# Kernel optimization log

Measured on AMD Instinct MI355X. Metric: run time of the kernel, lower is better.

The kernel has to match this reference:

```python
import jax, jax.numpy as jnp
import numpy as np

B, D, O, K = 8192, 256, 256, 16


def setup_inputs() -> dict:
    key = jax.random.key(0)
    k1, k2, k3, k4 = jax.random.split(key, 4)
    x = jax.random.normal(k1, (B, D), dtype=jnp.float32)
    # learned params
    values = jax.random.uniform(k2, (O, D, K), dtype=jnp.float32, minval=-0.05, maxval=0.05)
    skip_w = jax.random.normal(k3, (O, D), dtype=jnp.float32) * (1.0 / np.sqrt(D))
    skip_b = jax.random.uniform(k4, (O,), dtype=jnp.float32, minval=-1.0, maxval=1.0) / np.sqrt(D)
    # fixed buffer (non-trainable)
    grid = jnp.linspace(-1.0, 1.0, K).astype(jnp.float32)
    return {"x": x, "values": values, "skip_w": skip_w, "skip_b": skip_b, "grid": grid}


def reference(x, values, skip_w, skip_b, grid):
    # x: [B, D]; values: [O, D, K]; grid: [K]
    num_knots = grid.shape[0]
    xc = jnp.clip(x, -1.0, 1.0)
    # torch.bucketize(x, grid) (right=False) == searchsorted side='left'
    right = jnp.searchsorted(grid, xc, side="left")            # [B, D]
    left = jnp.clip(right - 1, 0, num_knots - 2)               # [B, D]
    right = left + 1
    g0 = grid[left]
    g1 = grid[right]
    w = (xc - g0) / (g1 - g0 + 1e-12)                          # [B, D]
    # sparse linear-interp coefficients over knots: 2 nonzeros per (b, d)
    coeff = (1.0 - w)[..., None] * jax.nn.one_hot(left, num_knots, dtype=xc.dtype) \
          + w[..., None] * jax.nn.one_hot(right, num_knots, dtype=xc.dtype)  # [B, D, K]
    # y[b,o] = sum_d sum_k coeff[b,d,k] * values[o,d,k]  (== per-dim gather+interp+accumulate)
    y = jnp.einsum("bdk,odk->bo", coeff, values)
    y = y + xc @ skip_w.T + skip_b
    return y
```

## Files before the change

kernel.cpp:

```cpp
#include <hip/hip_runtime.h>
#include <hip/hip_bf16.h>
#include <stdint.h>


#define D_DIM  256
#define O_DIM  256
#define KK     4096
#define BM     64
#define BN     64
#define BK     128
#define NT     (KK / BK)
#define NTHREADS 256

typedef __attribute__((ext_vector_type(8))) short bf16x8;
typedef __attribute__((ext_vector_type(4))) float f32x4;

__global__ __launch_bounds__(256) void kan_prep(
    const float* __restrict__ values,
    const float* __restrict__ skip_w,
    const float* __restrict__ gknots,
    unsigned short* __restrict__ Vp)
{
    int tid = blockIdx.x * blockDim.x + threadIdx.x;
    int e = tid * 8;
    int o = e >> 12;
    int kflat = e & 4095;
    int od = (o << 8) | (kflat >> 4);
    float sw = skip_w[od];
    int kmod = kflat & 15;

    const float4* vp4 = reinterpret_cast<const float4*>(values + e);
    float4 v0 = vp4[0], v1 = vp4[1];
    float f[8] = {v0.x, v0.y, v0.z, v0.w, v1.x, v1.y, v1.z, v1.w};
    unsigned int w[4];
#pragma unroll
    for (int j = 0; j < 4; ++j) {
        float2 ab;
        ab.x = f[2*j]     + gknots[kmod + 2*j]     * sw;
        ab.y = f[2*j + 1] + gknots[kmod + 2*j + 1] * sw;
        __hip_bfloat162 p2 = __float22bfloat162_rn(ab);
        __builtin_memcpy(&w[j], &p2, 4);
    }

    int cblk = o >> 6, n = o & 63;
    int kt = kflat >> 7;
    int k8 = (kflat >> 3) & 15;
    int slot = n * 16 + (k8 ^ (n & 7));
    size_t dst = (((size_t)(cblk * NT + kt)) * 1024 + (size_t)slot) * 8;
    *reinterpret_cast<uint4*>(Vp + dst) = make_uint4(w[0], w[1], w[2], w[3]);
}

__global__ __launch_bounds__(NTHREADS, 2) void kan_gemm(
    const float* __restrict__ x,
    const unsigned short* __restrict__ Vp,
    const float* __restrict__ skip_b,
    float* __restrict__ out)
{
    __shared__ unsigned short As[2][BM * BK];
    __shared__ unsigned short Bs[2][BN * BK];

    const int t    = threadIdx.x;
    const int lane = t & 63;
    const int wid  = t >> 6;
    const int wm   = wid >> 1;
    const int wn   = wid & 1;
    const int l15  = lane & 15;
    const int lhi  = lane >> 4;

    const int bm0  = (int)(blockIdx.x >> 2) * BM;
    const int cblk = (int)(blockIdx.x & 3);
    const int oc0  = cblk * BN;

    const int ab  = t >> 2;
    const int adl = t & 3;
    const float* xp = x + (size_t)(bm0 + ab) * D_DIM + adl;

    char* arow0 = (char*)&As[0][0] + ab * 256;
    char* arow1 = (char*)&As[1][0] + ab * 256;
    const int cs0 = ((2 * adl)     ^ (ab & 7)) * 16;
    const int cs1 = ((2 * adl + 1) ^ (ab & 7)) * 16;
    const int cs2 = ((2 * adl + 8) ^ (ab & 7)) * 16;
    const int cs3 = ((2 * adl + 9) ^ (ab & 7)) * 16;

    f32x4 acc[2][2] = {};

    auto buildwd = [&](float xv, unsigned int* wd) {
        float xc = fminf(1.f, fmaxf(-1.f, xv));
        float tt = (xc + 1.f) * 7.5f;
        int li = (int)tt;
        li = li > 14 ? 14 : li;
        float w1 = tt - (float)li;
        float2 cw; cw.x = 1.f - w1; cw.y = w1;
        __hip_bfloat162 p2 = __float22bfloat162_rn(cw);
        unsigned int pk;
        __builtin_memcpy(&pk, &p2, 4);
        unsigned long long w64 = (unsigned long long)pk << ((li & 1) * 16);
        unsigned int lo = (unsigned int)w64;
        unsigned int hi = (unsigned int)(w64 >> 32);
        int jl = li >> 1;
#pragma unroll
        for (int j = 0; j < 8; ++j)
            wd[j] = (j == jl) ? lo : ((j == jl + 1) ? hi : 0u);
    };

    auto stageA = [&](char* arow, float xv0, float xv1) {
        unsigned int wd[8];
        buildwd(xv0, wd);
        *reinterpret_cast<uint4*>(arow + cs0) = make_uint4(wd[0], wd[1], wd[2], wd[3]);
        *reinterpret_cast<uint4*>(arow + cs1) = make_uint4(wd[4], wd[5], wd[6], wd[7]);
        buildwd(xv1, wd);
        *reinterpret_cast<uint4*>(arow + cs2) = make_uint4(wd[0], wd[1], wd[2], wd[3]);
        *reinterpret_cast<uint4*>(arow + cs3) = make_uint4(wd[4], wd[5], wd[6], wd[7]);
    };

    auto stageB = [&](int buf, int ktile) {
        const char* tb = (const char*)(Vp + ((size_t)(cblk * NT + ktile)) * (BN * BK));
        char* lb = (char*)&Bs[buf][0];
#pragma unroll
        for (int r = 0; r < 4; ++r) {
            const char* g = tb + (r * 256 + t) * 16;
            unsigned ldsoff = (unsigned)((r * 256 + wid * 64) * 16);
            __builtin_amdgcn_global_load_lds(
                (const __attribute__((address_space(1))) unsigned int*)g,
                (__attribute__((address_space(3))) unsigned int*)(lb + ldsoff),
                16, 0, 0);
        }
    };

    float xn0 = xp[0], xn1 = xp[4];
    stageB(0, 0);
    stageA(arow0, xn0, xn1);
    xn0 = xp[8]; xn1 = xp[12];
    __syncthreads();

    for (int kt = 0; kt < NT; ++kt) {
        const int cur = kt & 1;

        if (kt + 1 < NT) stageB(cur ^ 1, kt + 1);

        bf16x8 af[2][4], bg[2][4];
        const char* Ab = (const char*)&As[cur][0];
        const char* Bb = (const char*)&Bs[cur][0];
#pragma unroll
        for (int kh = 0; kh < 4; ++kh) {
            int k8 = kh * 4 + lhi;
#pragma unroll
            for (int mi = 0; mi < 2; ++mi) {
                int m = wm * 32 + mi * 16 + l15;
                af[mi][kh] = *reinterpret_cast<const bf16x8*>(
                    Ab + m * 256 + ((k8 ^ (m & 7)) * 16));
            }
#pragma unroll
            for (int ni = 0; ni < 2; ++ni) {
                int n = wn * 32 + ni * 16 + l15;
                bg[ni][kh] = *reinterpret_cast<const bf16x8*>(
                    Bb + n * 256 + ((k8 ^ (n & 7)) * 16));
            }
        }

        if (kt + 1 < NT) {
            stageA(cur ? arow0 : arow1, xn0, xn1);
            if (kt + 2 < NT) {
                xn0 = xp[(kt + 2) * 8];
                xn1 = xp[(kt + 2) * 8 + 4];
            }
        }

#pragma unroll
        for (int mi = 0; mi < 2; ++mi)
#pragma unroll
            for (int ni = 0; ni < 2; ++ni)
#pragma unroll
                for (int kh = 0; kh < 4; ++kh)
                    acc[mi][ni] = __builtin_amdgcn_mfma_f32_16x16x32_bf16(
                        af[mi][kh], bg[ni][kh], acc[mi][ni], 0, 0, 0);

        __syncthreads();
    }

#pragma unroll
    for (int ni = 0; ni < 2; ++ni) {
        int col = oc0 + wn * 32 + ni * 16 + l15;
        float sb = skip_b[col];
#pragma unroll
        for (int mi = 0; mi < 2; ++mi) {
            f32x4 v = acc[mi][ni];
            int row0 = bm0 + wm * 32 + mi * 16 + lhi * 4;
#pragma unroll
            for (int r = 0; r < 4; ++r)
                out[(size_t)(row0 + r) * O_DIM + col] = v[r] + sb;
        }
    }
}

extern "C" void kernel_launch(void* const* d_in, const int* in_sizes, int n_in,
                              void* d_out, int out_size, void* d_ws, size_t ws_size,
                              hipStream_t stream) {
    const float* x      = (const float*)d_in[0];
    const float* values = (const float*)d_in[1];
    const float* skip_w = (const float*)d_in[2];
    const float* skip_b = (const float*)d_in[3];
    const float* gknots = (const float*)d_in[4];
    float* out = (float*)d_out;
    unsigned short* Vp = (unsigned short*)d_ws;

    kan_prep<<<dim3(512), dim3(256), 0, stream>>>(values, skip_w, gknots, Vp);

    kan_gemm<<<dim3(512), dim3(NTHREADS), 0, stream>>>(x, Vp, skip_b, out);
}
```

Before: 49.02 us.

## Use 128x128 tiles with 4-way split-K and atomic output accumulation

Enlarges the GEMM block tile from 64x64 to 128x128 with a BK of 64, and splits the 4096-long reduction across 4 blocks per output tile. Partial sums are combined with float atomics into an output zeroed by a memset, and only the first split adds the bias. The larger tile raises operand reuse per LDS load, and split-K keeps the grid at 512 blocks. The cost is an extra memset, atomic traffic on the 8 MB output, non-deterministic summation order, and higher register pressure from the 4x4 accumulator array.

```diff
diff --git a/kernel.cpp b/kernel.cpp
--- a/kernel.cpp
+++ b/kernel.cpp
@@ -5,11 +5,11 @@
 
 #define D_DIM  256
 #define O_DIM  256
-#define KK     4096
-#define BM     64
-#define BN     64
-#define BK     128
-#define NT     (KK / BK)
+#define BM     128
+#define BN     128
+#define BK     64
+#define KSPLIT 4
+#define ITERS  16
 #define NTHREADS 256
 
 typedef __attribute__((ext_vector_type(8))) short bf16x8;
@@ -25,8 +25,7 @@
     int e = tid * 8;
     int o = e >> 12;
     int kflat = e & 4095;
-    int od = (o << 8) | (kflat >> 4);
-    float sw = skip_w[od];
+    float sw = skip_w[(o << 8) | (kflat >> 4)];
     int kmod = kflat & 15;
 
     const float4* vp4 = reinterpret_cast<const float4*>(values + e);
@@ -42,15 +41,14 @@
         __builtin_memcpy(&w[j], &p2, 4);
     }
 
-    int cblk = o >> 6, n = o & 63;
-    int kt = kflat >> 7;
-    int k8 = (kflat >> 3) & 15;
-    int slot = n * 16 + (k8 ^ (n & 7));
-    size_t dst = (((size_t)(cblk * NT + kt)) * 1024 + (size_t)slot) * 8;
+    int ntile = o >> 7, n = o & 127;
+    int kt = kflat >> 6, k8 = (kflat >> 3) & 7;
+    int slot = n * 8 + (k8 ^ (n & 7));
+    size_t dst = ((size_t)(ntile * 64 + kt) * 1024 + (size_t)slot) * 8;
     *reinterpret_cast<uint4*>(Vp + dst) = make_uint4(w[0], w[1], w[2], w[3]);
 }
 
-__global__ __launch_bounds__(NTHREADS, 2) void kan_gemm(
+__global__ __launch_bounds__(NTHREADS) void kan_gemm(
     const float* __restrict__ x,
     const unsigned short* __restrict__ Vp,
     const float* __restrict__ skip_b,
@@ -67,22 +65,25 @@
     const int l15  = lane & 15;
     const int lhi  = lane >> 4;
 
-    const int bm0  = (int)(blockIdx.x >> 2) * BM;
-    const int cblk = (int)(blockIdx.x & 3);
-    const int oc0  = cblk * BN;
-
-    const int ab  = t >> 2;
-    const int adl = t & 3;
-    const float* xp = x + (size_t)(bm0 + ab) * D_DIM + adl;
-
-    char* arow0 = (char*)&As[0][0] + ab * 256;
-    char* arow1 = (char*)&As[1][0] + ab * 256;
-    const int cs0 = ((2 * adl)     ^ (ab & 7)) * 16;
-    const int cs1 = ((2 * adl + 1) ^ (ab & 7)) * 16;
-    const int cs2 = ((2 * adl + 8) ^ (ab & 7)) * 16;
-    const int cs3 = ((2 * adl + 9) ^ (ab & 7)) * 16;
-
-    f32x4 acc[2][2] = {};
+    const int bid = (int)blockIdx.x;
+    const int ks  = bid & 3;
+    const int nt  = (bid >> 2) & 1;
+    const int mt  = bid >> 3;
+    const int bm0 = mt * BM;
+    const int oc0 = nt * BN;
+    const int kt0 = ks * ITERS;
+
+    const int ab  = t >> 1;
+    const int ad2 = (t & 1) * 2;
+    const float* xp = x + (size_t)(bm0 + ab) * D_DIM + ks * 64 + ad2;
+
+    char* arow[2] = { (char*)&As[0][0] + ab * 128, (char*)&As[1][0] + ab * 128 };
+    const int cs0 = ((ad2 * 2)     ^ (ab & 7)) * 16;
+    const int cs1 = ((ad2 * 2 + 1) ^ (ab & 7)) * 16;
+    const int cs2 = ((ad2 * 2 + 2) ^ (ab & 7)) * 16;
+    const int cs3 = ((ad2 * 2 + 3) ^ (ab & 7)) * 16;
+
+    f32x4 acc[4][4] = {};
 
     auto buildwd = [&](float xv, unsigned int* wd) {
         float xc = fminf(1.f, fmaxf(-1.f, xv));
@@ -103,18 +104,19 @@
             wd[j] = (j == jl) ? lo : ((j == jl + 1) ? hi : 0u);
     };
 
-    auto stageA = [&](char* arow, float xv0, float xv1) {
+    auto stageA = [&](int buf, float xv0, float xv1) {
         unsigned int wd[8];
+        char* a = arow[buf];
         buildwd(xv0, wd);
-        *reinterpret_cast<uint4*>(arow + cs0) = make_uint4(wd[0], wd[1], wd[2], wd[3]);
-        *reinterpret_cast<uint4*>(arow + cs1) = make_uint4(wd[4], wd[5], wd[6], wd[7]);
+        *reinterpret_cast<uint4*>(a + cs0) = make_uint4(wd[0], wd[1], wd[2], wd[3]);
+        *reinterpret_cast<uint4*>(a + cs1) = make_uint4(wd[4], wd[5], wd[6], wd[7]);
         buildwd(xv1, wd);
-        *reinterpret_cast<uint4*>(arow + cs2) = make_uint4(wd[0], wd[1], wd[2], wd[3]);
-        *reinterpret_cast<uint4*>(arow + cs3) = make_uint4(wd[4], wd[5], wd[6], wd[7]);
+        *reinterpret_cast<uint4*>(a + cs2) = make_uint4(wd[0], wd[1], wd[2], wd[3]);
+        *reinterpret_cast<uint4*>(a + cs3) = make_uint4(wd[4], wd[5], wd[6], wd[7]);
     };
 
-    auto stageB = [&](int buf, int ktile) {
-        const char* tb = (const char*)(Vp + ((size_t)(cblk * NT + ktile)) * (BN * BK));
+    auto stageB = [&](int buf, int ktg) {
+        const char* tb = (const char*)(Vp + ((size_t)(nt * 64 + ktg)) * 8192);
         char* lb = (char*)&Bs[buf][0];
 #pragma unroll
         for (int r = 0; r < 4; ++r) {
@@ -127,51 +129,49 @@
         }
     };
 
-    float xn0 = xp[0], xn1 = xp[4];
-    stageB(0, 0);
-    stageA(arow0, xn0, xn1);
-    xn0 = xp[8]; xn1 = xp[12];
+    float2 xn = *reinterpret_cast<const float2*>(xp);
+    stageB(0, kt0);
+    stageA(0, xn.x, xn.y);
+    xn = *reinterpret_cast<const float2*>(xp + 4);
     __syncthreads();
 
-    for (int kt = 0; kt < NT; ++kt) {
+    for (int kt = 0; kt < ITERS; ++kt) {
         const int cur = kt & 1;
 
-        if (kt + 1 < NT) stageB(cur ^ 1, kt + 1);
-
-        bf16x8 af[2][4], bg[2][4];
+        if (kt + 1 < ITERS) stageB(cur ^ 1, kt0 + kt + 1);
+
+        bf16x8 af[4][2], bg[4][2];
         const char* Ab = (const char*)&As[cur][0];
         const char* Bb = (const char*)&Bs[cur][0];
 #pragma unroll
-        for (int kh = 0; kh < 4; ++kh) {
+        for (int kh = 0; kh < 2; ++kh) {
             int k8 = kh * 4 + lhi;
 #pragma unroll
-            for (int mi = 0; mi < 2; ++mi) {
-                int m = wm * 32 + mi * 16 + l15;
+            for (int mi = 0; mi < 4; ++mi) {
+                int m = wm * 64 + mi * 16 + l15;
                 af[mi][kh] = *reinterpret_cast<const bf16x8*>(
-                    Ab + m * 256 + ((k8 ^ (m & 7)) * 16));
+                    Ab + m * 128 + ((k8 ^ (m & 7)) * 16));
             }
 #pragma unroll
-            for (int ni = 0; ni < 2; ++ni) {
-                int n = wn * 32 + ni * 16 + l15;
+            for (int ni = 0; ni < 4; ++ni) {
+                int n = wn * 64 + ni * 16 + l15;
                 bg[ni][kh] = *reinterpret_cast<const bf16x8*>(
-                    Bb + n * 256 + ((k8 ^ (n & 7)) * 16));
+                    Bb + n * 128 + ((k8 ^ (n & 7)) * 16));
             }
         }
 
-        if (kt + 1 < NT) {
-            stageA(cur ? arow0 : arow1, xn0, xn1);
-            if (kt + 2 < NT) {
-                xn0 = xp[(kt + 2) * 8];
-                xn1 = xp[(kt + 2) * 8 + 4];
-            }
-        }
-
-#pragma unroll
-        for (int mi = 0; mi < 2; ++mi)
-#pragma unroll
-            for (int ni = 0; ni < 2; ++ni)
-#pragma unroll
-                for (int kh = 0; kh < 4; ++kh)
+        if (kt + 1 < ITERS) {
+            stageA(cur ^ 1, xn.x, xn.y);
+            if (kt + 2 < ITERS)
+                xn = *reinterpret_cast<const float2*>(xp + (kt + 2) * 4);
+        }
+
+#pragma unroll
+        for (int mi = 0; mi < 4; ++mi)
+#pragma unroll
+            for (int ni = 0; ni < 4; ++ni)
+#pragma unroll
+                for (int kh = 0; kh < 2; ++kh)
                     acc[mi][ni] = __builtin_amdgcn_mfma_f32_16x16x32_bf16(
                         af[mi][kh], bg[ni][kh], acc[mi][ni], 0, 0, 0);
 
@@ -179,16 +179,16 @@
     }
 
 #pragma unroll
-    for (int ni = 0; ni < 2; ++ni) {
-        int col = oc0 + wn * 32 + ni * 16 + l15;
-        float sb = skip_b[col];
-#pragma unroll
-        for (int mi = 0; mi < 2; ++mi) {
+    for (int ni = 0; ni < 4; ++ni) {
+        int col = oc0 + wn * 64 + ni * 16 + l15;
+        float sb = (ks == 0) ? skip_b[col] : 0.f;
+#pragma unroll
+        for (int mi = 0; mi < 4; ++mi) {
             f32x4 v = acc[mi][ni];
-            int row0 = bm0 + wm * 32 + mi * 16 + lhi * 4;
+            int row0 = bm0 + wm * 64 + mi * 16 + lhi * 4;
 #pragma unroll
             for (int r = 0; r < 4; ++r)
-                out[(size_t)(row0 + r) * O_DIM + col] = v[r] + sb;
+                unsafeAtomicAdd(&out[(size_t)(row0 + r) * O_DIM + col], v[r] + sb);
         }
     }
 }
@@ -203,6 +203,9 @@
     const float* gknots = (const float*)d_in[4];
     float* out = (float*)d_out;
     unsigned short* Vp = (unsigned short*)d_ws;
+    (void)in_sizes; (void)n_in; (void)out_size; (void)ws_size;
+
+    hipMemsetAsync(out, 0, (size_t)8192 * 256 * sizeof(float), stream);
 
     kan_prep<<<dim3(512), dim3(256), 0, stream>>>(values, skip_w, gknots, Vp);
 
```

Result: slower. 59.23 us (+20.8%).
